# Kernel tuning notes

Measured on AMD Instinct MI355X. Metric: run time of the kernel, lower is better.

Reference implementation:

```python
import jax, jax.numpy as jnp
import numpy as np

DIM = 1024
HEADS = 16
DIM_HEAD = 64
INNER = HEADS * DIM_HEAD  # 1024


def setup_inputs() -> dict:
    key = jax.random.key(0)
    kx, kqkv, kwo, kbo = jax.random.split(key, 4)
    x = jax.random.normal(kx, (4, 2048, DIM), dtype=jnp.float32)
    # nn.Linear weights stored as [out, in]; we keep [in, out] for x @ W
    w_qkv = jax.random.normal(kqkv, (DIM, 3 * INNER), dtype=jnp.float32) * (1.0 / np.sqrt(DIM))
    w_out = jax.random.normal(kwo, (INNER, DIM), dtype=jnp.float32) * (1.0 / np.sqrt(INNER))
    b_out = jax.random.normal(kbo, (DIM,), dtype=jnp.float32) * 0.01
    return {"x": x, "w_qkv": w_qkv, "w_out": w_out, "b_out": b_out}


def reference(x, w_qkv, w_out, b_out):
    b, n, _ = x.shape
    scale = 1.0 / np.sqrt(DIM_HEAD)
    qkv = x @ w_qkv  # [b, n, 3*inner]
    q, k, v = jnp.split(qkv, 3, axis=-1)
    # [b, n, inner] -> [b, h, n, d]
    reshape = lambda z: z.reshape(b, n, HEADS, DIM_HEAD).transpose(0, 2, 1, 3)
    q, k, v = reshape(q), reshape(k), reshape(v)
    sim = jnp.einsum('bhid,bhjd->bhij', q, k) * scale
    attn = jax.nn.softmax(sim, axis=-1)  # dropout p=0.0 -> identity
    out = jnp.einsum('bhij,bhjd->bhid', attn, v)
    out = out.transpose(0, 2, 1, 3).reshape(b, n, INNER)
    return out @ w_out + b_out
```

## Files before the change

### kernel.cpp

```cpp
#include <hip/hip_runtime.h>
#include <hip/hip_fp16.h>

typedef __attribute__((ext_vector_type(4))) float f32x4;
typedef __attribute__((ext_vector_type(8))) _Float16 h8;
typedef __attribute__((ext_vector_type(4))) _Float16 h4;

__device__ __forceinline__ void gld16(const _Float16* g, _Float16* l) {
  __builtin_amdgcn_global_load_lds(
      (const __attribute__((address_space(1))) void*)g,
      (__attribute__((address_space(3))) void*)l, 16, 0, 0);
}

__global__ void cvt_f32_h(const float* __restrict__ in, _Float16* __restrict__ out, int n8) {
  for (int i = blockIdx.x * blockDim.x + threadIdx.x; i < n8; i += gridDim.x * blockDim.x) {
    const f32x4* p = (const f32x4*)(in + (size_t)i * 8);
    f32x4 a = p[0], b = p[1];
    h8 o;
    o[0] = (_Float16)a[0]; o[1] = (_Float16)a[1]; o[2] = (_Float16)a[2]; o[3] = (_Float16)a[3];
    o[4] = (_Float16)b[0]; o[5] = (_Float16)b[1]; o[6] = (_Float16)b[2]; o[7] = (_Float16)b[3];
    *(h8*)(out + (size_t)i * 8) = o;
  }
}

__global__ void transpose_cvt(const float* __restrict__ in, _Float16* __restrict__ out, int R, int C) {
  __shared__ float tile[32][33];
  const int tx = threadIdx.x & 31, ty = threadIdx.x >> 5;
  const int c = blockIdx.x * 32 + tx;
#pragma unroll
  for (int j = 0; j < 32; j += 8) {
    int r = blockIdx.y * 32 + ty + j;
    tile[ty + j][tx] = in[(size_t)r * C + c];
  }
  __syncthreads();
#pragma unroll
  for (int j = 0; j < 32; j += 8) {
    out[(size_t)(blockIdx.x * 32 + ty + j) * R + blockIdx.y * 32 + tx] = (_Float16)tile[tx][ty + j];
  }
}

template <int EPI>
__global__ __launch_bounds__(256, 2)
void gemm_kernel(const _Float16* __restrict__ A, const _Float16* __restrict__ Bt,
                 float* __restrict__ outF, const float* __restrict__ bias,
                 _Float16* __restrict__ q_h, _Float16* __restrict__ k_h,
                 _Float16* __restrict__ v_t, const int Nn, const int K) {
  __shared__ _Float16 As[128 * 64];
  __shared__ _Float16 Bs[128 * 64];
  const int tid = threadIdx.x;
  const int wid = tid >> 6, lane = tid & 63;
  const int g = lane >> 4, r16 = lane & 15;
  const int wr = wid >> 1, wc = wid & 1;
  const int row0 = blockIdx.x * 128;
  const int col0 = blockIdx.y * 128;
  f32x4 acc[4][4] = {};
  const int sr = tid >> 3, sc = tid & 7;
  const _Float16* ag = A + (size_t)(row0 + sr) * K + sc * 8;
  const _Float16* bg = Bt + (size_t)(col0 + sr) * K + sc * 8;

  for (int kt = 0; kt < K; kt += 64) {
    __syncthreads();
#pragma unroll
    for (int i = 0; i < 4; ++i)
      gld16(ag + (size_t)i * 32 * K + kt, As + i * 2048 + wid * 512);
#pragma unroll
    for (int i = 0; i < 4; ++i)
      gld16(bg + (size_t)i * 32 * K + kt, Bs + i * 2048 + wid * 512);
    __syncthreads();

#pragma unroll
    for (int kk = 0; kk < 2; ++kk) {
      h8 af[4], bf[4];
#pragma unroll
      for (int mt = 0; mt < 4; ++mt)
        af[mt] = *(const h8*)(As + (wr * 64 + mt * 16 + r16) * 64 + kk * 32 + g * 8);
#pragma unroll
      for (int nt = 0; nt < 4; ++nt)
        bf[nt] = *(const h8*)(Bs + (wc * 64 + nt * 16 + r16) * 64 + kk * 32 + g * 8);
#pragma unroll
      for (int mt = 0; mt < 4; ++mt)
#pragma unroll
        for (int nt = 0; nt < 4; ++nt)
          acc[mt][nt] = __builtin_amdgcn_mfma_f32_16x16x32_f16(af[mt], bf[nt], acc[mt][nt], 0, 0, 0);
    }
  }

  if (EPI == 0) {
    const float qscale = 0.125f * 1.44269504088896340736f;
#pragma unroll
    for (int mt = 0; mt < 4; ++mt) {
#pragma unroll
      for (int nt = 0; nt < 4; ++nt) {
        const int j = col0 + wc * 64 + nt * 16 + r16;
        const int which = j >> 10;
        const int hd = j & 1023;
        const int hh = hd >> 6, dd = hd & 63;
#pragma unroll
        for (int rg = 0; rg < 4; ++rg) {
          const int mm = row0 + wr * 64 + mt * 16 + g * 4 + rg;
          const int b = mm >> 11, n = mm & 2047;
          const size_t bh = (size_t)(b * 16 + hh);
          const float v = acc[mt][nt][rg];
          if (which == 0)      q_h[(bh * 2048 + n) * 64 + dd] = (_Float16)(v * qscale);
          else if (which == 1) k_h[(bh * 2048 + n) * 64 + dd] = (_Float16)v;
          else                 v_t[(bh * 64 + dd) * 2048 + n] = (_Float16)v;
        }
      }
    }
  } else {
#pragma unroll
    for (int mt = 0; mt < 4; ++mt) {
#pragma unroll
      for (int nt = 0; nt < 4; ++nt) {
        const int j = col0 + wc * 64 + nt * 16 + r16;
        const float bv = bias[j];
#pragma unroll
        for (int rg = 0; rg < 4; ++rg) {
          const int mm = row0 + wr * 64 + mt * 16 + g * 4 + rg;
          outF[(size_t)mm * Nn + j] = acc[mt][nt][rg] + bv;
        }
      }
    }
  }
}

__global__ __launch_bounds__(256, 2)
void attn_kernel(const _Float16* __restrict__ Qall, const _Float16* __restrict__ Kall,
                 const _Float16* __restrict__ Vtall, _Float16* __restrict__ Oall) {
  __shared__ _Float16 Qs[64 * 64];
  __shared__ _Float16 Ks[64 * 64];
  __shared__ _Float16 Vs[64 * 64];
  const int tid = threadIdx.x;
  const int wid = tid >> 6, lane = tid & 63;
  const int g = lane >> 4, r16 = lane & 15;
  const int blk = blockIdx.x;
  const int qt = blk & 31;
  const int bh = blk >> 5;
  const _Float16* Qg = Qall + (size_t)bh * (2048 * 64);
  const _Float16* Kg = Kall + (size_t)bh * (2048 * 64);
  const _Float16* Vg = Vtall + (size_t)bh * (2048 * 64);
  const int q0 = qt * 64;
  const int sr = tid >> 3, sc = tid & 7;

#pragma unroll
  for (int i = 0; i < 2; ++i) {
    int r = i * 32 + sr;
    gld16(Qg + (size_t)(q0 + r) * 64 + ((sc ^ (r & 7)) << 3), Qs + i * 2048 + wid * 512);
  }
  __syncthreads();

  const int qrow = wid * 16 + r16;
  const int qsw = qrow & 7;
  const h8 qf0 = *(const h8*)(Qs + qrow * 64 + ((g ^ qsw) << 3));
  const h8 qf1 = *(const h8*)(Qs + qrow * 64 + (((g + 4) ^ qsw) << 3));

  f32x4 ot[4] = {};
  float m = -3.0e38f, lsum = 0.f;

  for (int t = 0; t < 32; ++t) {
    const int kv0 = t * 64;
    __syncthreads();
#pragma unroll
    for (int i = 0; i < 2; ++i) {
      int r = i * 32 + sr;
      gld16(Kg + (size_t)(kv0 + r) * 64 + ((sc ^ (r & 7)) << 3), Ks + i * 2048 + wid * 512);
    }
#pragma unroll
    for (int i = 0; i < 2; ++i) {
      int r = i * 32 + sr;
      gld16(Vg + (size_t)r * 2048 + kv0 + ((sc ^ (r & 7)) << 3), Vs + i * 2048 + wid * 512);
    }
    __syncthreads();

    f32x4 st[4];
#pragma unroll
    for (int f = 0; f < 4; ++f) {
      const int krow = f * 16 + r16;
      const int ks = krow & 7;
      h8 ka0 = *(const h8*)(Ks + krow * 64 + ((g ^ ks) << 3));
      h8 ka1 = *(const h8*)(Ks + krow * 64 + (((g + 4) ^ ks) << 3));
      f32x4 s = {};
      s = __builtin_amdgcn_mfma_f32_16x16x32_f16(ka0, qf0, s, 0, 0, 0);
      s = __builtin_amdgcn_mfma_f32_16x16x32_f16(ka1, qf1, s, 0, 0, 0);
      st[f] = s;
    }

    float pmax = st[0][0];
#pragma unroll
    for (int f = 0; f < 4; ++f)
#pragma unroll
      for (int rg = 0; rg < 4; ++rg) pmax = fmaxf(pmax, st[f][rg]);
    pmax = fmaxf(pmax, __shfl_xor(pmax, 16));
    pmax = fmaxf(pmax, __shfl_xor(pmax, 32));
    const float mnew = fmaxf(m, pmax);
    const float corr = __builtin_amdgcn_exp2f(m - mnew);
    m = mnew;
    float rs = 0.f;
    h4 pb[4];
#pragma unroll
    for (int f = 0; f < 4; ++f) {
#pragma unroll
      for (int rg = 0; rg < 4; ++rg) {
        float p = __builtin_amdgcn_exp2f(st[f][rg] - mnew);
        rs += p;
        pb[f][rg] = (_Float16)p;
      }
    }
    rs += __shfl_xor(rs, 16);
    rs += __shfl_xor(rs, 32);
    lsum = lsum * corr + rs;
#pragma unroll
    for (int db = 0; db < 4; ++db) ot[db] *= corr;

#pragma unroll
    for (int db = 0; db < 4; ++db) {
      const int vrow = db * 16 + r16;
      const int vs_ = (vrow & 7) << 3;
#pragma unroll
      for (int f = 0; f < 4; ++f) {
        h4 va = *(const h4*)(Vs + vrow * 64 + ((f * 16 + g * 4) ^ vs_));
        ot[db] = __builtin_amdgcn_mfma_f32_16x16x16f16(va, pb[f], ot[db], 0, 0, 0);
      }
    }
  }

  const float inv = 1.f / lsum;
  __syncthreads();
  _Float16* olds = Ks;
#pragma unroll
  for (int db = 0; db < 4; ++db)
#pragma unroll
    for (int rg = 0; rg < 4; ++rg) {
      const int d = db * 16 + g * 4 + rg;
      olds[qrow * 64 + (d ^ ((qrow & 7) << 3))] = (_Float16)(ot[db][rg] * inv);
    }
  __syncthreads();
  const int bb = bh >> 4, hh = bh & 15;
#pragma unroll
  for (int i = 0; i < 2; ++i) {
    const int idx = tid + i * 256;
    const int q = idx >> 3, c = idx & 7;
    h8 vv = *(const h8*)(olds + q * 64 + ((c ^ (q & 7)) << 3));
    *(h8*)(Oall + ((size_t)(bb * 2048 + q0 + q) * 1024 + hh * 64 + c * 8)) = vv;
  }
}

extern "C" void kernel_launch(void* const* d_in, const int* in_sizes, int n_in,
                              void* d_out, int out_size, void* d_ws, size_t ws_size,
                              hipStream_t stream) {
  const float* x     = (const float*)d_in[0];
  const float* w_qkv = (const float*)d_in[1];
  const float* w_out = (const float*)d_in[2];
  const float* b_out = (const float*)d_in[3];
  float* out = (float*)d_out;

  char* ws = (char*)d_ws;
  _Float16* x_h    = (_Float16*)(ws);
  _Float16* wqkv_t = (_Float16*)(ws + 16777216);
  _Float16* wout_t = (_Float16*)(ws + 23068672);
  _Float16* q_h    = (_Float16*)(ws + 25165824);
  _Float16* k_h    = (_Float16*)(ws + 41943040);
  _Float16* v_t    = (_Float16*)(ws + 58720256);
  _Float16* o_h    = (_Float16*)(ws + 75497472);

  hipLaunchKernelGGL(cvt_f32_h, dim3(2048), dim3(256), 0, stream, x, x_h, (8192 * 1024) / 8);
  hipLaunchKernelGGL(transpose_cvt, dim3(96, 32), dim3(256), 0, stream, w_qkv, wqkv_t, 1024, 3072);
  hipLaunchKernelGGL(transpose_cvt, dim3(32, 32), dim3(256), 0, stream, w_out, wout_t, 1024, 1024);

  hipLaunchKernelGGL((gemm_kernel<0>), dim3(64, 24), dim3(256), 0, stream,
                     x_h, wqkv_t, nullptr, nullptr, q_h, k_h, v_t, 3072, 1024);

  hipLaunchKernelGGL(attn_kernel, dim3(2048), dim3(256), 0, stream, q_h, k_h, v_t, o_h);

  hipLaunchKernelGGL((gemm_kernel<1>), dim3(64, 8), dim3(256), 0, stream,
                     o_h, wout_t, out, b_out, nullptr, nullptr, nullptr, 1024, 1024);
}
```

Before: 255.2 us.

## Enlarge attention query tile, double-buffer K/V, and add lazy softmax rescaling

The attention kernel now gives each block 256 query rows (64 per wave, four 16-row sub-blocks) instead of 64. Each K/V tile is therefore loaded into shared memory once and reused across four times more queries. K/V staging is double-buffered so the next tile's async global-to-LDS load overlaps compute on the current one. Block IDs are remapped so blocks of the same head are spread out, and the running max is rescaled only when it grows by more than a threshold. The trade-offs are much higher register pressure (64 accumulator floats plus fragments per lane), a quarter as many blocks (512) and more LDS per block, which may lower occupancy.

New measurement: 224.1 us. 1.14x faster.

```diff
diff --git a/kernel.cpp b/kernel.cpp
--- a/kernel.cpp
+++ b/kernel.cpp
@@ -123,123 +123,150 @@
   }
 }
 
+__device__ __forceinline__ void stage_kv(const _Float16* Kg, const _Float16* Vg,
+                                         _Float16* KsB, _Float16* VsB,
+                                         int kv0, int sr, int sc8, int wid) {
+#pragma unroll
+  for (int i = 0; i < 2; ++i) {
+    int r = i * 32 + sr;
+    gld16(Kg + (size_t)(kv0 + r) * 64 + (sc8 ^ ((r & 7) * 8)), KsB + i * 2048 + wid * 512);
+    gld16(Vg + (size_t)r * 2048 + kv0 + (sc8 ^ ((r & 7) * 8)), VsB + i * 2048 + wid * 512);
+  }
+}
+
 __global__ __launch_bounds__(256, 2)
 void attn_kernel(const _Float16* __restrict__ Qall, const _Float16* __restrict__ Kall,
                  const _Float16* __restrict__ Vtall, _Float16* __restrict__ Oall) {
-  __shared__ _Float16 Qs[64 * 64];
-  __shared__ _Float16 Ks[64 * 64];
-  __shared__ _Float16 Vs[64 * 64];
+  __shared__ _Float16 Qs[256 * 64];
+  __shared__ _Float16 Ks[2][64 * 64];
+  __shared__ _Float16 Vs[2][64 * 64];
   const int tid = threadIdx.x;
   const int wid = tid >> 6, lane = tid & 63;
   const int g = lane >> 4, r16 = lane & 15;
-  const int blk = blockIdx.x;
-  const int qt = blk & 31;
-  const int bh = blk >> 5;
+  const int blk = (blockIdx.x & 7) * 64 + (blockIdx.x >> 3);
+  const int qt = blk & 7;
+  const int bh = blk >> 3;
   const _Float16* Qg = Qall + (size_t)bh * (2048 * 64);
   const _Float16* Kg = Kall + (size_t)bh * (2048 * 64);
   const _Float16* Vg = Vtall + (size_t)bh * (2048 * 64);
-  const int q0 = qt * 64;
-  const int sr = tid >> 3, sc = tid & 7;
-
-#pragma unroll
-  for (int i = 0; i < 2; ++i) {
+  const int q0 = qt * 256;
+  const int sr = tid >> 3, sc8 = (tid & 7) * 8;
+
+#pragma unroll
+  for (int i = 0; i < 8; ++i) {
     int r = i * 32 + sr;
-    gld16(Qg + (size_t)(q0 + r) * 64 + ((sc ^ (r & 7)) << 3), Qs + i * 2048 + wid * 512);
-  }
+    gld16(Qg + (size_t)(q0 + r) * 64 + (sc8 ^ ((r & 7) * 8)), Qs + i * 2048 + wid * 512);
+  }
+  stage_kv(Kg, Vg, Ks[0], Vs[0], 0, sr, sc8, wid);
   __syncthreads();
 
-  const int qrow = wid * 16 + r16;
-  const int qsw = qrow & 7;
-  const h8 qf0 = *(const h8*)(Qs + qrow * 64 + ((g ^ qsw) << 3));
-  const h8 qf1 = *(const h8*)(Qs + qrow * 64 + (((g + 4) ^ qsw) << 3));
-
-  f32x4 ot[4] = {};
-  float m = -3.0e38f, lsum = 0.f;
-
-  for (int t = 0; t < 32; ++t) {
-    const int kv0 = t * 64;
-    __syncthreads();
-#pragma unroll
-    for (int i = 0; i < 2; ++i) {
-      int r = i * 32 + sr;
-      gld16(Kg + (size_t)(kv0 + r) * 64 + ((sc ^ (r & 7)) << 3), Ks + i * 2048 + wid * 512);
-    }
-#pragma unroll
-    for (int i = 0; i < 2; ++i) {
-      int r = i * 32 + sr;
-      gld16(Vg + (size_t)r * 2048 + kv0 + ((sc ^ (r & 7)) << 3), Vs + i * 2048 + wid * 512);
-    }
-    __syncthreads();
-
-    f32x4 st[4];
-#pragma unroll
-    for (int f = 0; f < 4; ++f) {
-      const int krow = f * 16 + r16;
-      const int ks = krow & 7;
-      h8 ka0 = *(const h8*)(Ks + krow * 64 + ((g ^ ks) << 3));
-      h8 ka1 = *(const h8*)(Ks + krow * 64 + (((g + 4) ^ ks) << 3));
-      f32x4 s = {};
-      s = __builtin_amdgcn_mfma_f32_16x16x32_f16(ka0, qf0, s, 0, 0, 0);
-      s = __builtin_amdgcn_mfma_f32_16x16x32_f16(ka1, qf1, s, 0, 0, 0);
-      st[f] = s;
-    }
-
-    float pmax = st[0][0];
-#pragma unroll
-    for (int f = 0; f < 4; ++f)
-#pragma unroll
-      for (int rg = 0; rg < 4; ++rg) pmax = fmaxf(pmax, st[f][rg]);
-    pmax = fmaxf(pmax, __shfl_xor(pmax, 16));
-    pmax = fmaxf(pmax, __shfl_xor(pmax, 32));
-    const float mnew = fmaxf(m, pmax);
-    const float corr = __builtin_amdgcn_exp2f(m - mnew);
-    m = mnew;
-    float rs = 0.f;
-    h4 pb[4];
-#pragma unroll
-    for (int f = 0; f < 4; ++f) {
-#pragma unroll
-      for (int rg = 0; rg < 4; ++rg) {
-        float p = __builtin_amdgcn_exp2f(st[f][rg] - mnew);
-        rs += p;
-        pb[f][rg] = (_Float16)p;
-      }
-    }
-    rs += __shfl_xor(rs, 16);
-    rs += __shfl_xor(rs, 32);
-    lsum = lsum * corr + rs;
-#pragma unroll
-    for (int db = 0; db < 4; ++db) ot[db] *= corr;
-
+  h8 qf[4][2];
+#pragma unroll
+  for (int qb = 0; qb < 4; ++qb) {
+    const int qrow = wid * 64 + qb * 16 + r16;
+#pragma unroll
+    for (int kd = 0; kd < 2; ++kd)
+      qf[qb][kd] = *(const h8*)(Qs + qrow * 64 + ((kd * 32 + g * 8) ^ ((qrow & 7) * 8)));
+  }
+
+  f32x4 ot[4][4] = {};
+  float m[4], l[4];
+#pragma unroll
+  for (int qb = 0; qb < 4; ++qb) { m[qb] = -3.0e38f; l[qb] = 0.f; }
+
+  auto compute = [&](const _Float16* KsB, const _Float16* VsB) {
+    h8 kf[4][2];
+#pragma unroll
+    for (int kb = 0; kb < 4; ++kb) {
+      const int krow = kb * 16 + r16;
+#pragma unroll
+      for (int kd = 0; kd < 2; ++kd)
+        kf[kb][kd] = *(const h8*)(KsB + krow * 64 + ((kd * 32 + g * 8) ^ ((krow & 7) * 8)));
+    }
+    h4 vf[4][4];
 #pragma unroll
     for (int db = 0; db < 4; ++db) {
       const int vrow = db * 16 + r16;
-      const int vs_ = (vrow & 7) << 3;
-#pragma unroll
-      for (int f = 0; f < 4; ++f) {
-        h4 va = *(const h4*)(Vs + vrow * 64 + ((f * 16 + g * 4) ^ vs_));
-        ot[db] = __builtin_amdgcn_mfma_f32_16x16x16f16(va, pb[f], ot[db], 0, 0, 0);
+#pragma unroll
+      for (int kg = 0; kg < 4; ++kg)
+        vf[db][kg] = *(const h4*)(VsB + vrow * 64 + ((kg * 16 + g * 4) ^ ((vrow & 7) * 8)));
+    }
+#pragma unroll
+    for (int qb = 0; qb < 4; ++qb) {
+      f32x4 st[4];
+#pragma unroll
+      for (int kb = 0; kb < 4; ++kb) {
+        f32x4 s = {};
+        s = __builtin_amdgcn_mfma_f32_16x16x32_f16(kf[kb][0], qf[qb][0], s, 0, 0, 0);
+        s = __builtin_amdgcn_mfma_f32_16x16x32_f16(kf[kb][1], qf[qb][1], s, 0, 0, 0);
+        st[kb] = s;
       }
-    }
-  }
-
-  const float inv = 1.f / lsum;
-  __syncthreads();
-  _Float16* olds = Ks;
-#pragma unroll
-  for (int db = 0; db < 4; ++db)
-#pragma unroll
-    for (int rg = 0; rg < 4; ++rg) {
-      const int d = db * 16 + g * 4 + rg;
-      olds[qrow * 64 + (d ^ ((qrow & 7) << 3))] = (_Float16)(ot[db][rg] * inv);
-    }
+      float pmax = st[0][0];
+#pragma unroll
+      for (int kb = 0; kb < 4; ++kb)
+#pragma unroll
+        for (int rg = 0; rg < 4; ++rg) pmax = fmaxf(pmax, st[kb][rg]);
+      pmax = fmaxf(pmax, __shfl_xor(pmax, 16));
+      pmax = fmaxf(pmax, __shfl_xor(pmax, 32));
+      if (__any(pmax > m[qb] + 8.f)) {
+        const float mn = fmaxf(m[qb], pmax);
+        const float corr = __builtin_amdgcn_exp2f(m[qb] - mn);
+        l[qb] *= corr;
+#pragma unroll
+        for (int db = 0; db < 4; ++db) ot[qb][db] *= corr;
+        m[qb] = mn;
+      }
+      float rs = 0.f;
+      h4 pb[4];
+#pragma unroll
+      for (int kb = 0; kb < 4; ++kb)
+#pragma unroll
+        for (int rg = 0; rg < 4; ++rg) {
+          float p = __builtin_amdgcn_exp2f(st[kb][rg] - m[qb]);
+          rs += p;
+          pb[kb][rg] = (_Float16)p;
+        }
+      rs += __shfl_xor(rs, 16);
+      rs += __shfl_xor(rs, 32);
+      l[qb] += rs;
+#pragma unroll
+      for (int db = 0; db < 4; ++db)
+#pragma unroll
+        for (int kg = 0; kg < 4; ++kg)
+          ot[qb][db] = __builtin_amdgcn_mfma_f32_16x16x16f16(vf[db][kg], pb[kg], ot[qb][db], 0, 0, 0);
+    }
+  };
+
+#pragma unroll 1
+  for (int tt = 0; tt < 16; ++tt) {
+    stage_kv(Kg, Vg, Ks[1], Vs[1], (tt * 2 + 1) * 64, sr, sc8, wid);
+    compute(Ks[0], Vs[0]);
+    __syncthreads();
+    if (tt < 15) stage_kv(Kg, Vg, Ks[0], Vs[0], (tt * 2 + 2) * 64, sr, sc8, wid);
+    compute(Ks[1], Vs[1]);
+    __syncthreads();
+  }
+
+#pragma unroll
+  for (int qb = 0; qb < 4; ++qb) {
+    const float inv = 1.f / l[qb];
+    const int qrow = wid * 64 + qb * 16 + r16;
+    const int x = (qrow & 7) * 8;
+#pragma unroll
+    for (int db = 0; db < 4; ++db) {
+      h4 o;
+#pragma unroll
+      for (int rg = 0; rg < 4; ++rg) o[rg] = (_Float16)(ot[qb][db][rg] * inv);
+      *(h4*)(Qs + qrow * 64 + ((db * 16 + g * 4) ^ x)) = o;
+    }
+  }
   __syncthreads();
   const int bb = bh >> 4, hh = bh & 15;
 #pragma unroll
-  for (int i = 0; i < 2; ++i) {
+  for (int i = 0; i < 8; ++i) {
     const int idx = tid + i * 256;
     const int q = idx >> 3, c = idx & 7;
-    h8 vv = *(const h8*)(olds + q * 64 + ((c ^ (q & 7)) << 3));
+    h8 vv = *(const h8*)(Qs + q * 64 + ((c * 8) ^ ((q & 7) * 8)));
     *(h8*)(Oall + ((size_t)(bb * 2048 + q0 + q) * 1024 + hh * 64 + c * 8)) = vv;
   }
 }
@@ -269,7 +296,7 @@
   hipLaunchKernelGGL((gemm_kernel<0>), dim3(64, 24), dim3(256), 0, stream,
                      x_h, wqkv_t, nullptr, nullptr, q_h, k_h, v_t, 3072, 1024);
 
-  hipLaunchKernelGGL(attn_kernel, dim3(2048), dim3(256), 0, stream, q_h, k_h, v_t, o_h);
+  hipLaunchKernelGGL(attn_kernel, dim3(512), dim3(256), 0, stream, q_h, k_h, v_t, o_h);
 
   hipLaunchKernelGGL((gemm_kernel<1>), dim3(64, 8), dim3(256), 0, stream,
                      o_h, wout_t, out, b_out, nullptr, nullptr, nullptr, 1024, 1024);
```
